# Performance work log

Hardware: AMD Instinct MI355X
Metric: run time of the kernel (lower is better)

The kernel has to match this reference:

```python
import jax, jax.numpy as jnp
import numpy as np

CHANNELS = 8
IN_CHANNELS = 8
NUM_LAYERS = 3
MASK_OUT_STRIDE = 2
SOI = jnp.array([64.0, 128.0, 256.0, 512.0, 1024.0], dtype=jnp.float32)
WEIGHT_NUMS = [(IN_CHANNELS + 2) * CHANNELS, CHANNELS * CHANNELS, CHANNELS * 1]
BIAS_NUMS = [CHANNELS, CHANNELS, 1]


def mish(x):
    return x * jnp.tanh(jax.nn.softplus(x))


def compute_locations(h, w, stride):
    # matches AdelaiDet compute_locations: (x, y) centers at stride*i + stride//2
    ys = jnp.arange(h, dtype=jnp.float32) * stride + stride // 2
    xs = jnp.arange(w, dtype=jnp.float32) * stride + stride // 2
    yy, xx = jnp.meshgrid(ys, xs, indexing='ij')
    return jnp.stack([xx.ravel(), yy.ravel()], axis=-1)  # [H*W, 2]


def _axis_interp(x, in_size, out_size, factor, axis):
    # out[y] = bilinear sample of x at coord max(y - factor//2, 0)/factor (align_corners=True grid)
    coords = jnp.maximum(jnp.arange(out_size) - factor // 2, 0) / factor
    i0 = jnp.floor(coords).astype(jnp.int32)
    i1 = jnp.minimum(i0 + 1, in_size - 1)
    frac = (coords - i0).astype(x.dtype)
    x0 = jnp.take(x, i0, axis=axis)
    x1 = jnp.take(x, i1, axis=axis)
    shp = [1] * x.ndim
    shp[axis] = out_size
    frac = frac.reshape(shp)
    return x0 * (1 - frac) + x1 * frac


def aligned_bilinear(t, factor):
    # faithful to AdelaiDet aligned_bilinear: edge-pad (0,1,0,1), align_corners
    # interpolate to (factor*h+1, factor*w+1), edge-pad front by factor//2, crop.
    if factor == 1:
        return t
    n, c, h, w = t.shape
    tp = jnp.pad(t, ((0, 0), (0, 0), (0, 1), (0, 1)), mode='edge')
    tp = _axis_interp(tp, h + 1, factor * h, factor, axis=2)
    tp = _axis_interp(tp, w + 1, factor * w, factor, axis=3)
    return tp


def parse_dynamic_params(params, n_inst):
    offs = np.cumsum([0] + WEIGHT_NUMS + BIAS_NUMS)
    ws, bs = [], []
    for l in range(NUM_LAYERS):
        out_ch = CHANNELS if l < NUM_LAYERS - 1 else 1
        ws.append(params[:, offs[l]:offs[l + 1]].reshape(n_inst, out_ch, -1))
        bs.append(params[:, offs[NUM_LAYERS + l]:offs[NUM_LAYERS + l + 1]].reshape(n_inst, out_ch))
    return ws, bs


def setup_inputs() -> dict:
    key = jax.random.key(0)
    k1, k2, k3, k4, k5 = jax.random.split(key, 5)
    N, H, W, n_inst = 2, 100, 152, 100
    return {
        'mask_feats': jax.random.normal(k1, (N, IN_CHANNELS, H, W), dtype=jnp.float32),
        'mask_head_params': jax.random.normal(k2, (n_inst, 169), dtype=jnp.float32),
        'instance_locations': jax.random.uniform(k3, (n_inst, 2), dtype=jnp.float32) * 800.0,
        'im_inds': jax.random.randint(k4, (n_inst,), 0, N, dtype=jnp.int32),
        'fpn_levels': jax.random.randint(k5, (n_inst,), 0, 5, dtype=jnp.int32),
        'mask_feat_stride': 8,
    }


def reference(mask_feats, mask_head_params, instance_locations, im_inds, fpn_levels, mask_feat_stride):
    N, Cin, H, W = mask_feats.shape
    n_inst = mask_head_params.shape[0]
    locs = compute_locations(H, W, mask_feat_stride)                     # [HW, 2]
    rel = instance_locations[:, None, :] - locs[None, :, :]             # [n, HW, 2]
    rel = jnp.transpose(rel, (0, 2, 1))                                  # [n, 2, HW]
    soi = SOI[fpn_levels]                                                # [n]
    rel = rel / soi[:, None, None]
    feats = mask_feats[im_inds].reshape(n_inst, Cin, H * W)              # gather per instance
    x = jnp.concatenate([rel, feats], axis=1)                            # [n, Cin+2, HW]
    ws, bs = parse_dynamic_params(mask_head_params, n_inst)
    for l, (w, b) in enumerate(zip(ws, bs)):
        # grouped 1x1 conv with groups=n_inst == per-instance matmul
        x = jnp.einsum('noi,nip->nop', w, x) + b[:, :, None]
        if l < NUM_LAYERS - 1:
            x = mish(x)
    logits = x.reshape(n_inst, 1, H, W)
    factor = int(mask_feat_stride) // MASK_OUT_STRIDE
    logits = aligned_bilinear(logits, factor)
    return jax.nn.sigmoid(logits)
```

## Files before the change

kernel.cpp:

```cpp
#include <hip/hip_runtime.h>


#define CIN 8
#define HH 100
#define WW 152
#define HWSZ (HH * WW)
#define NI 100
#define OH (HH * 4)
#define OW (WW * 4)
#define TROWS 10
#define LROWS (TROWS + 2)
#define QPR (WW / 4)
#define NQUADS (LROWS * QPR)
#define UITEMS (TROWS * WW)
#define BLOCK 512

__device__ __forceinline__ float fast_rcp(float x) {
    return __builtin_amdgcn_rcpf(x);
}

__device__ __forceinline__ float fast_mish(float x) {
    float e = __expf(fminf(x, 20.f));
    float n = e * (e + 2.f);
    return x * n * fast_rcp(n + 2.f);
}

__device__ __forceinline__ float fast_sigmoid(float z) {
    return fast_rcp(1.f + __expf(-z));
}

__global__ void __launch_bounds__(BLOCK, 2)
fused_mask_head_kernel(const float* __restrict__ mask_feats,
                       const float* __restrict__ params,
                       const float* __restrict__ inst_locs,
                       const int* __restrict__ im_inds,
                       const int* __restrict__ fpn_levels,
                       const int* __restrict__ stride_ptr,
                       float* __restrict__ out) {
    __shared__ float prm[169];
    __shared__ float tile[LROWS][WW];

    const int inst = blockIdx.y;
    const int r0 = blockIdx.x * TROWS;
    const int t = threadIdx.x;

    if (t < 169) prm[t] = params[inst * 169 + t];
    __syncthreads();

    const int stride = stride_ptr[0];
    const float half = (float)(stride / 2);
    const float soi_tab[5] = {64.f, 128.f, 256.f, 512.f, 1024.f};
    const float inv_soi = 1.f / soi_tab[fpn_levels[inst]];
    const float lx = inst_locs[inst * 2 + 0];
    const float ly = inst_locs[inst * 2 + 1];
    const float dx = -(float)stride * inv_soi;
    const float* fbase = mask_feats + (size_t)im_inds[inst] * CIN * HWSZ;

    if (t < NQUADS) {
        const int lr  = t / QPR;
        const int qc  = t - lr * QPR;
        const int col = qc * 4;
        const int gr  = min(max(r0 + lr - 1, 0), HH - 1);

        const float relY = (ly - (float)(gr * stride) - half) * inv_soi;
        const float x0b  = (lx - (float)(col * stride) - half) * inv_soi;

        const float* fb = fbase + gr * WW + col;
        float4 f[CIN];
#pragma unroll
        for (int c = 0; c < CIN; ++c)
            f[c] = *reinterpret_cast<const float4*>(fb + (size_t)c * HWSZ);
#define FEAT(c, j) ((&f[c].x)[(j)])

        float h1[8][4];
#pragma unroll
        for (int o = 0; o < 8; ++o) {
            float w[10];
#pragma unroll
            for (int i = 0; i < 10; ++i) w[i] = prm[o * 10 + i];
            const float b = prm[152 + o];
#pragma unroll
            for (int j = 0; j < 4; ++j) {
                float acc = fmaf(w[0], x0b + (float)j * dx, fmaf(w[1], relY, b));
#pragma unroll
                for (int c = 0; c < CIN; ++c) acc = fmaf(w[2 + c], FEAT(c, j), acc);
                h1[o][j] = fast_mish(acc);
            }
        }
        float lo[4];
        const float b3 = prm[168];
#pragma unroll
        for (int j = 0; j < 4; ++j) lo[j] = b3;
#pragma unroll
        for (int o = 0; o < 8; ++o) {
            float w[8];
#pragma unroll
            for (int i = 0; i < 8; ++i) w[i] = prm[80 + o * 8 + i];
            const float b2 = prm[160 + o];
            const float w3 = prm[144 + o];
#pragma unroll
            for (int j = 0; j < 4; ++j) {
                float acc = b2;
#pragma unroll
                for (int i = 0; i < 8; ++i) acc = fmaf(w[i], h1[i][j], acc);
                lo[j] = fmaf(w3, fast_mish(acc), lo[j]);
            }
        }
        *reinterpret_cast<float4*>(&tile[lr][col]) = make_float4(lo[0], lo[1], lo[2], lo[3]);
#undef FEAT
    }
    __syncthreads();

    for (int b = t; b < UITEMS; b += BLOCK) {
        const int rg = b / WW;
        const int cg = b - rg * WW;
        const int lr = rg + 1;
        const int gm1 = max(cg - 1, 0), gp1 = min(cg + 1, WW - 1);

        const float v00 = tile[lr - 1][gm1], v01 = tile[lr - 1][cg], v02 = tile[lr - 1][gp1];
        const float v10 = tile[lr    ][gm1], v11 = tile[lr    ][cg], v12 = tile[lr    ][gp1];
        const float v20 = tile[lr + 1][gm1], v21 = tile[lr + 1][cg], v22 = tile[lr + 1][gp1];

        float h0[4], h1[4], h2[4];
        h0[0] = 0.5f * (v00 + v01); h0[1] = fmaf(0.25f, v00, 0.75f * v01); h0[2] = v01; h0[3] = fmaf(0.25f, v02, 0.75f * v01);
        h1[0] = 0.5f * (v10 + v11); h1[1] = fmaf(0.25f, v10, 0.75f * v11); h1[2] = v11; h1[3] = fmaf(0.25f, v12, 0.75f * v11);
        h2[0] = 0.5f * (v20 + v21); h2[1] = fmaf(0.25f, v20, 0.75f * v21); h2[2] = v21; h2[3] = fmaf(0.25f, v22, 0.75f * v21);

        float* O = out + (size_t)inst * (OH * OW) + (size_t)(4 * (r0 + rg)) * OW + 4 * cg;
        float4 row;
        row.x = fast_sigmoid(0.5f * (h0[0] + h1[0]));
        row.y = fast_sigmoid(0.5f * (h0[1] + h1[1]));
        row.z = fast_sigmoid(0.5f * (h0[2] + h1[2]));
        row.w = fast_sigmoid(0.5f * (h0[3] + h1[3]));
        *reinterpret_cast<float4*>(O) = row;
        row.x = fast_sigmoid(fmaf(0.25f, h0[0], 0.75f * h1[0]));
        row.y = fast_sigmoid(fmaf(0.25f, h0[1], 0.75f * h1[1]));
        row.z = fast_sigmoid(fmaf(0.25f, h0[2], 0.75f * h1[2]));
        row.w = fast_sigmoid(fmaf(0.25f, h0[3], 0.75f * h1[3]));
        *reinterpret_cast<float4*>(O + OW) = row;
        row.x = fast_sigmoid(h1[0]);
        row.y = fast_sigmoid(h1[1]);
        row.z = fast_sigmoid(h1[2]);
        row.w = fast_sigmoid(h1[3]);
        *reinterpret_cast<float4*>(O + 2 * OW) = row;
        row.x = fast_sigmoid(fmaf(0.25f, h2[0], 0.75f * h1[0]));
        row.y = fast_sigmoid(fmaf(0.25f, h2[1], 0.75f * h1[1]));
        row.z = fast_sigmoid(fmaf(0.25f, h2[2], 0.75f * h1[2]));
        row.w = fast_sigmoid(fmaf(0.25f, h2[3], 0.75f * h1[3]));
        *reinterpret_cast<float4*>(O + 3 * OW) = row;
    }
}

extern "C" void kernel_launch(void* const* d_in, const int* in_sizes, int n_in,
                              void* d_out, int out_size, void* d_ws, size_t ws_size,
                              hipStream_t stream) {
    const float* mask_feats = (const float*)d_in[0];
    const float* params     = (const float*)d_in[1];
    const float* inst_locs  = (const float*)d_in[2];
    const int*   im_inds    = (const int*)d_in[3];
    const int*   fpn_levels = (const int*)d_in[4];
    const int*   stride_ptr = (const int*)d_in[5];
    float* out = (float*)d_out;

    dim3 block(BLOCK);
    dim3 grid(HH / TROWS, NI);
    fused_mask_head_kernel<<<grid, block, 0, stream>>>(
        mask_feats, params, inst_locs, im_inds, fpn_levels, stride_ptr, out);
}
```

Measured before the change: 31.15 us.

## Replace shared-memory tile with wave-shuffle row streaming per column

Each thread now owns one column and walks down the rows of its tile sequentially, prefetching the next row's features. Horizontal neighbours come from wave shuffles, and vertical neighbours from a three-row register window. This removes the shared-memory logits tile and the second barrier, and overlaps the feature loads with compute. In exchange, each block has fewer threads (192), some lanes are wasted on halo and padding columns, and each thread runs a longer serial loop.

Result: slower. 48.92 us (+57.0%).

```diff
diff --git a/kernel.cpp b/kernel.cpp
--- a/kernel.cpp
+++ b/kernel.cpp
@@ -8,12 +8,8 @@
 #define NI 100
 #define OH (HH * 4)
 #define OW (WW * 4)
-#define TROWS 10
-#define LROWS (TROWS + 2)
-#define QPR (WW / 4)
-#define NQUADS (LROWS * QPR)
-#define UITEMS (TROWS * WW)
-#define BLOCK 512
+#define TR 10
+#define BLOCK 192
 
 __device__ __forceinline__ float fast_rcp(float x) {
     return __builtin_amdgcn_rcpf(x);
@@ -29,7 +25,7 @@
     return fast_rcp(1.f + __expf(-z));
 }
 
-__global__ void __launch_bounds__(BLOCK, 2)
+__global__ void __launch_bounds__(BLOCK)
 fused_mask_head_kernel(const float* __restrict__ mask_feats,
                        const float* __restrict__ params,
                        const float* __restrict__ inst_locs,
@@ -38,14 +34,17 @@
                        const int* __restrict__ stride_ptr,
                        float* __restrict__ out) {
     __shared__ float prm[169];
-    __shared__ float tile[LROWS][WW];
-
     const int inst = blockIdx.y;
-    const int r0 = blockIdx.x * TROWS;
+    const int r0 = blockIdx.x * TR;
     const int t = threadIdx.x;
-
     if (t < 169) prm[t] = params[inst * 169 + t];
     __syncthreads();
+
+    const int wave = t >> 6;
+    const int lane = t & 63;
+    const int c = wave * 62 + lane - 1;
+    const int colc = min(max(c, 0), WW - 1);
+    const bool emit_ok = (lane >= 1) && (lane <= 62) && (c >= 0) && (c < WW);
 
     const int stride = stride_ptr[0];
     const float half = (float)(stride / 2);
@@ -53,101 +52,91 @@
     const float inv_soi = 1.f / soi_tab[fpn_levels[inst]];
     const float lx = inst_locs[inst * 2 + 0];
     const float ly = inst_locs[inst * 2 + 1];
-    const float dx = -(float)stride * inv_soi;
-    const float* fbase = mask_feats + (size_t)im_inds[inst] * CIN * HWSZ;
+    const float xrel = (lx - (float)(colc * stride) - half) * inv_soi;
+    const float* fcol = mask_feats + (size_t)im_inds[inst] * CIN * HWSZ + colc;
+    float* const obase = out + (size_t)inst * (OH * OW);
 
-    if (t < NQUADS) {
-        const int lr  = t / QPR;
-        const int qc  = t - lr * QPR;
-        const int col = qc * 4;
-        const int gr  = min(max(r0 + lr - 1, 0), HH - 1);
+    float pl = 0.f, pm = 0.f, prr = 0.f;
+    float clft = 0.f, cm = 0.f, crt = 0.f;
+    float nl = 0.f, nm = 0.f, nr = 0.f;
 
-        const float relY = (ly - (float)(gr * stride) - half) * inv_soi;
-        const float x0b  = (lx - (float)(col * stride) - half) * inv_soi;
+    float f[CIN], fn[CIN];
+    {
+        const int rr = min(max(r0 - 1, 0), HH - 1);
+        const float* fr = fcol + rr * WW;
+#pragma unroll
+        for (int ch = 0; ch < CIN; ++ch) f[ch] = fr[(size_t)ch * HWSZ];
+    }
 
-        const float* fb = fbase + gr * WW + col;
-        float4 f[CIN];
+    for (int i = 0; i < TR + 2; ++i) {
+        const int rU = r0 + i - 1;
+        const int rr = min(max(rU, 0), HH - 1);
+
+        if (i < TR + 1) {
+            const int rn = min(max(rU + 1, 0), HH - 1);
+            const float* fr = fcol + rn * WW;
 #pragma unroll
-        for (int c = 0; c < CIN; ++c)
-            f[c] = *reinterpret_cast<const float4*>(fb + (size_t)c * HWSZ);
-#define FEAT(c, j) ((&f[c].x)[(j)])
+            for (int ch = 0; ch < CIN; ++ch) fn[ch] = fr[(size_t)ch * HWSZ];
+        }
 
-        float h1[8][4];
+        const float relY = (ly - (float)(rr * stride) - half) * inv_soi;
+        float h1[8];
 #pragma unroll
         for (int o = 0; o < 8; ++o) {
-            float w[10];
+            float acc = fmaf(prm[o * 10 + 0], xrel, fmaf(prm[o * 10 + 1], relY, prm[152 + o]));
 #pragma unroll
-            for (int i = 0; i < 10; ++i) w[i] = prm[o * 10 + i];
-            const float b = prm[152 + o];
-#pragma unroll
-            for (int j = 0; j < 4; ++j) {
-                float acc = fmaf(w[0], x0b + (float)j * dx, fmaf(w[1], relY, b));
-#pragma unroll
-                for (int c = 0; c < CIN; ++c) acc = fmaf(w[2 + c], FEAT(c, j), acc);
-                h1[o][j] = fast_mish(acc);
-            }
+            for (int ch = 0; ch < CIN; ++ch) acc = fmaf(prm[o * 10 + 2 + ch], f[ch], acc);
+            h1[o] = fast_mish(acc);
         }
-        float lo[4];
-        const float b3 = prm[168];
-#pragma unroll
-        for (int j = 0; j < 4; ++j) lo[j] = b3;
+        float L = prm[168];
 #pragma unroll
         for (int o = 0; o < 8; ++o) {
-            float w[8];
+            float acc = prm[160 + o];
 #pragma unroll
-            for (int i = 0; i < 8; ++i) w[i] = prm[80 + o * 8 + i];
-            const float b2 = prm[160 + o];
-            const float w3 = prm[144 + o];
+            for (int ii = 0; ii < 8; ++ii) acc = fmaf(prm[80 + o * 8 + ii], h1[ii], acc);
+            L = fmaf(prm[144 + o], fast_mish(acc), L);
+        }
+
+        const float Ll = __shfl_up(L, 1);
+        const float Lr = __shfl_down(L, 1);
+
+        pl = clft; pm = cm; prr = crt;
+        clft = nl;  cm = nm;  crt = nr;
+        nl = Ll;  nm = L;   nr = Lr;
+
+        if (i >= 2 && emit_ok) {
+            const int rg = rU - 1;
+            float h0s[4], h1s[4], h2s[4];
+            h0s[0] = 0.5f * (pl + pm);  h0s[1] = fmaf(0.25f, pl, 0.75f * pm);  h0s[2] = pm; h0s[3] = fmaf(0.25f, prr, 0.75f * pm);
+            h1s[0] = 0.5f * (clft + cm); h1s[1] = fmaf(0.25f, clft, 0.75f * cm); h1s[2] = cm; h1s[3] = fmaf(0.25f, crt, 0.75f * cm);
+            h2s[0] = 0.5f * (nl + nm);  h2s[1] = fmaf(0.25f, nl, 0.75f * nm);  h2s[2] = nm; h2s[3] = fmaf(0.25f, nr, 0.75f * nm);
+
+            float* O = obase + (size_t)(4 * rg) * OW + 4 * c;
+            float4 row;
+            row.x = fast_sigmoid(0.5f * (h0s[0] + h1s[0]));
+            row.y = fast_sigmoid(0.5f * (h0s[1] + h1s[1]));
+            row.z = fast_sigmoid(0.5f * (h0s[2] + h1s[2]));
+            row.w = fast_sigmoid(0.5f * (h0s[3] + h1s[3]));
+            *reinterpret_cast<float4*>(O) = row;
+            row.x = fast_sigmoid(fmaf(0.25f, h0s[0], 0.75f * h1s[0]));
+            row.y = fast_sigmoid(fmaf(0.25f, h0s[1], 0.75f * h1s[1]));
+            row.z = fast_sigmoid(fmaf(0.25f, h0s[2], 0.75f * h1s[2]));
+            row.w = fast_sigmoid(fmaf(0.25f, h0s[3], 0.75f * h1s[3]));
+            *reinterpret_cast<float4*>(O + OW) = row;
+            row.x = fast_sigmoid(h1s[0]);
+            row.y = fast_sigmoid(h1s[1]);
+            row.z = fast_sigmoid(h1s[2]);
+            row.w = fast_sigmoid(h1s[3]);
+            *reinterpret_cast<float4*>(O + 2 * OW) = row;
+            row.x = fast_sigmoid(fmaf(0.25f, h2s[0], 0.75f * h1s[0]));
+            row.y = fast_sigmoid(fmaf(0.25f, h2s[1], 0.75f * h1s[1]));
+            row.z = fast_sigmoid(fmaf(0.25f, h2s[2], 0.75f * h1s[2]));
+            row.w = fast_sigmoid(fmaf(0.25f, h2s[3], 0.75f * h1s[3]));
+            *reinterpret_cast<float4*>(O + 3 * OW) = row;
+        }
+
 #pragma unroll
-            for (int j = 0; j < 4; ++j) {
-                float acc = b2;
-#pragma unroll
-                for (int i = 0; i < 8; ++i) acc = fmaf(w[i], h1[i][j], acc);
-                lo[j] = fmaf(w3, fast_mish(acc), lo[j]);
-            }
-        }
-        *reinterpret_cast<float4*>(&tile[lr][col]) = make_float4(lo[0], lo[1], lo[2], lo[3]);
-#undef FEAT
-    }
-    __syncthreads();
-
-    for (int b = t; b < UITEMS; b += BLOCK) {
-        const int rg = b / WW;
-        const int cg = b - rg * WW;
-        const int lr = rg + 1;
-        const int gm1 = max(cg - 1, 0), gp1 = min(cg + 1, WW - 1);
-
-        const float v00 = tile[lr - 1][gm1], v01 = tile[lr - 1][cg], v02 = tile[lr - 1][gp1];
-        const float v10 = tile[lr    ][gm1], v11 = tile[lr    ][cg], v12 = tile[lr    ][gp1];
-        const float v20 = tile[lr + 1][gm1], v21 = tile[lr + 1][cg], v22 = tile[lr + 1][gp1];
-
-        float h0[4], h1[4], h2[4];
-        h0[0] = 0.5f * (v00 + v01); h0[1] = fmaf(0.25f, v00, 0.75f * v01); h0[2] = v01; h0[3] = fmaf(0.25f, v02, 0.75f * v01);
-        h1[0] = 0.5f * (v10 + v11); h1[1] = fmaf(0.25f, v10, 0.75f * v11); h1[2] = v11; h1[3] = fmaf(0.25f, v12, 0.75f * v11);
-        h2[0] = 0.5f * (v20 + v21); h2[1] = fmaf(0.25f, v20, 0.75f * v21); h2[2] = v21; h2[3] = fmaf(0.25f, v22, 0.75f * v21);
-
-        float* O = out + (size_t)inst * (OH * OW) + (size_t)(4 * (r0 + rg)) * OW + 4 * cg;
-        float4 row;
-        row.x = fast_sigmoid(0.5f * (h0[0] + h1[0]));
-        row.y = fast_sigmoid(0.5f * (h0[1] + h1[1]));
-        row.z = fast_sigmoid(0.5f * (h0[2] + h1[2]));
-        row.w = fast_sigmoid(0.5f * (h0[3] + h1[3]));
-        *reinterpret_cast<float4*>(O) = row;
-        row.x = fast_sigmoid(fmaf(0.25f, h0[0], 0.75f * h1[0]));
-        row.y = fast_sigmoid(fmaf(0.25f, h0[1], 0.75f * h1[1]));
-        row.z = fast_sigmoid(fmaf(0.25f, h0[2], 0.75f * h1[2]));
-        row.w = fast_sigmoid(fmaf(0.25f, h0[3], 0.75f * h1[3]));
-        *reinterpret_cast<float4*>(O + OW) = row;
-        row.x = fast_sigmoid(h1[0]);
-        row.y = fast_sigmoid(h1[1]);
-        row.z = fast_sigmoid(h1[2]);
-        row.w = fast_sigmoid(h1[3]);
-        *reinterpret_cast<float4*>(O + 2 * OW) = row;
-        row.x = fast_sigmoid(fmaf(0.25f, h2[0], 0.75f * h1[0]));
-        row.y = fast_sigmoid(fmaf(0.25f, h2[1], 0.75f * h1[1]));
-        row.z = fast_sigmoid(fmaf(0.25f, h2[2], 0.75f * h1[2]));
-        row.w = fast_sigmoid(fmaf(0.25f, h2[3], 0.75f * h1[3]));
-        *reinterpret_cast<float4*>(O + 3 * OW) = row;
+        for (int ch = 0; ch < CIN; ++ch) f[ch] = fn[ch];
     }
 }
 
@@ -163,7 +152,7 @@
     float* out = (float*)d_out;
 
     dim3 block(BLOCK);
-    dim3 grid(HH / TROWS, NI);
+    dim3 grid(HH / TR, NI);
     fused_mask_head_kernel<<<grid, block, 0, stream>>>(
         mask_feats, params, inst_locs, im_inds, fpn_levels, stride_ptr, out);
 }
```
